# Optimization experiments

Hardware: AMD Instinct MI355X
Metric: run time of the kernel (lower is better)

Reference implementation:

```python
import jax, jax.numpy as jnp
import numpy as np
import math

HIDDEN_DIM = 1024
N_HEAD = 16
HEAD_DIM = HIDDEN_DIM // N_HEAD
BS, SEQ = 2, 4096


def setup_inputs() -> dict:
    key = jax.random.key(0)
    ks = jax.random.split(key, 6)
    s = 1.0 / math.sqrt(HIDDEN_DIM)
    return {
        "x": jax.random.normal(ks[0], (BS, SEQ, HIDDEN_DIM), dtype=jnp.float32),
        "attention_mask": jnp.zeros((1, 1, SEQ, SEQ), dtype=jnp.float32),
        "wq_w": jax.random.normal(ks[1], (HIDDEN_DIM, HIDDEN_DIM), dtype=jnp.float32) * s,
        "wq_b": jnp.zeros((HIDDEN_DIM,), dtype=jnp.float32),
        "wk_w": jax.random.normal(ks[2], (HIDDEN_DIM, HIDDEN_DIM), dtype=jnp.float32) * s,
        "wk_b": jnp.zeros((HIDDEN_DIM,), dtype=jnp.float32),
        "wv_w": jax.random.normal(ks[3], (HIDDEN_DIM, HIDDEN_DIM), dtype=jnp.float32) * s,
        "wv_b": jnp.zeros((HIDDEN_DIM,), dtype=jnp.float32),
        "wo_w": jax.random.normal(ks[4], (HIDDEN_DIM, HIDDEN_DIM), dtype=jnp.float32) * s,
        "wo_b": jnp.zeros((HIDDEN_DIM,), dtype=jnp.float32),
    }


def reference(x, attention_mask, wq_w, wq_b, wk_w, wk_b, wv_w, wv_b, wo_w, wo_b):
    bs, seq_len, _ = x.shape
    # nn.Linear: y = x @ W.T + b
    Q = x @ wq_w.T + wq_b
    K = x @ wk_w.T + wk_b
    V = x @ wv_w.T + wv_b
    # [bs, n_head, seq, head_dim]
    Q = Q.reshape(bs, seq_len, N_HEAD, HEAD_DIM).transpose(0, 2, 1, 3)
    K = K.reshape(bs, seq_len, N_HEAD, HEAD_DIM).transpose(0, 2, 1, 3)
    V = V.reshape(bs, seq_len, N_HEAD, HEAD_DIM).transpose(0, 2, 1, 3)
    scale = 1.0 / math.sqrt(HEAD_DIM)
    att = jnp.einsum('bhqd,bhkd->bhqk', Q, K) * scale
    att = att + attention_mask
    att = jax.nn.softmax(att, axis=-1)
    # dropout is identity in eval mode (p=0.1 during training)
    out = jnp.einsum('bhqk,bhkd->bhqd', att, V)
    out = out.transpose(0, 2, 1, 3).reshape(bs, seq_len, HIDDEN_DIM)
    return out @ wo_w.T + wo_b
```

## Files before the change

kernel.cpp:

```cpp
#include <hip/hip_runtime.h>

typedef unsigned short u16;
typedef __bf16 bf16x4 __attribute__((ext_vector_type(4)));
typedef __bf16 bf16x8 __attribute__((ext_vector_type(8)));
typedef float f32x4 __attribute__((ext_vector_type(4)));

#define SEQ_LEN 4096
#define HID 1024
#define NHEAD 16
#define HDIM 64
#define MROWS 8192
#define LOG2E 1.44269504088896f

__device__ __forceinline__ u16 f2bf(float f) {
  union { float f; unsigned u; } v; v.f = f;
  unsigned r = v.u + 0x7fffu + ((v.u >> 16) & 1u);
  return (u16)(r >> 16);
}

__device__ __forceinline__ float fexp2(float x) {
  float r;
  asm("v_exp_f32 %0, %1" : "=v"(r) : "v"(x));
  return r;
}

__device__ __forceinline__ void gload16(const void* g, void* lds) {
  __builtin_amdgcn_global_load_lds((const __attribute__((address_space(1))) void*)g,
                                   (__attribute__((address_space(3))) void*)lds, 16, 0, 0);
}


__global__ void cvt_x_kernel(const float* __restrict__ src, u16* __restrict__ dst, int n4) {
  int stride = gridDim.x * blockDim.x;
  for (int i = blockIdx.x * blockDim.x + threadIdx.x; i < n4; i += stride) {
    float4 v = ((const float4*)src)[i];
    ((ushort4*)dst)[i] = make_ushort4(f2bf(v.x), f2bf(v.y), f2bf(v.z), f2bf(v.w));
  }
}

__global__ void cvt_w_kernel(const float* __restrict__ w0, const float* __restrict__ w1,
                             const float* __restrict__ w2, const float* __restrict__ w3,
                             u16* __restrict__ dst) {
  const float* src = (blockIdx.y == 0) ? w0 : (blockIdx.y == 1) ? w1 : (blockIdx.y == 2) ? w2 : w3;
  u16* d = dst + (size_t)blockIdx.y * (HID * HID);
  int i = blockIdx.x * blockDim.x + threadIdx.x;
  float4 v = ((const float4*)src)[i];
  ((ushort4*)d)[i] = make_ushort4(f2bf(v.x), f2bf(v.y), f2bf(v.z), f2bf(v.w));
}

__global__ void maskchk_kernel(const float* __restrict__ mask, int n4, int* flag) {
  int stride = gridDim.x * blockDim.x;
  bool nz = false;
  for (int i = blockIdx.x * blockDim.x + threadIdx.x; i < n4; i += stride) {
    float4 v = ((const float4*)mask)[i];
    nz |= (v.x != 0.f) | (v.y != 0.f) | (v.z != 0.f) | (v.w != 0.f);
  }
  if (__any(nz) && (threadIdx.x & 63) == 0) atomicOr(flag, 1);
}


__device__ __forceinline__ void gemm_core(const u16* __restrict__ A, const u16* __restrict__ W,
                                          int m0, int n0, char* As, char* Bs, f32x4 acc[4][4]) {
  const int t = threadIdx.x, w = t >> 6, l = t & 63;
  const int lr = l & 15, lg = l >> 4;
  const int wr = (w >> 1) * 64, wc = (w & 1) * 64;
#pragma unroll
  for (int i = 0; i < 4; i++)
#pragma unroll
    for (int j = 0; j < 4; j++) acc[i][j] = (f32x4){0.f, 0.f, 0.f, 0.f};

  for (int k0 = 0; k0 < HID; k0 += 64) {
    __syncthreads();
#pragma unroll
    for (int j = 0; j < 4; j++) {
      int o = w * 4096 + j * 1024 + l * 16;
      int row = o >> 7, kb = (o >> 4) & 7, skb = kb ^ (row & 7);
      gload16(A + (size_t)(m0 + row) * HID + k0 + skb * 8, As + (w * 4096 + j * 1024));
      gload16(W + (size_t)(n0 + row) * HID + k0 + skb * 8, Bs + (w * 4096 + j * 1024));
    }
    __syncthreads();
#pragma unroll
    for (int ks = 0; ks < 2; ks++) {
      bf16x8 af[4], bf[4];
      int kb = ks * 4 + lg;
#pragma unroll
      for (int mt = 0; mt < 4; mt++) {
        int row = wr + mt * 16 + lr;
        af[mt] = *(const bf16x8*)(As + row * 128 + ((kb ^ (row & 7)) << 4));
      }
#pragma unroll
      for (int nt = 0; nt < 4; nt++) {
        int row = wc + nt * 16 + lr;
        bf[nt] = *(const bf16x8*)(Bs + row * 128 + ((kb ^ (row & 7)) << 4));
      }
#pragma unroll
      for (int mt = 0; mt < 4; mt++)
#pragma unroll
        for (int nt = 0; nt < 4; nt++)
          acc[mt][nt] = __builtin_amdgcn_mfma_f32_16x16x32_bf16(af[mt], bf[nt], acc[mt][nt], 0, 0, 0);
    }
  }
}

__global__ __launch_bounds__(256) void gemm_qkv_kernel(
    const u16* __restrict__ xb, const u16* __restrict__ wqb, const u16* __restrict__ wkb,
    const u16* __restrict__ wvb, const float* __restrict__ bq, const float* __restrict__ bk,
    const float* __restrict__ bv, u16* __restrict__ Qb, u16* __restrict__ Kb, u16* __restrict__ VT) {
  __shared__ __align__(128) char lds[32768];
  int m0 = blockIdx.x * 128;
  int ng = blockIdx.y * 128;
  int mat = ng >> 10, n0 = ng & 1023;
  const u16* W = (mat == 0) ? wqb : (mat == 1) ? wkb : wvb;
  const float* bias = (mat == 0) ? bq : (mat == 1) ? bk : bv;
  f32x4 acc[4][4];
  gemm_core(xb, W, m0, n0, lds, lds + 16384, acc);

  const int t = threadIdx.x, w = t >> 6, l = t & 63;
  const int lr = l & 15, lg = l >> 4;
  if (mat < 2) {
    u16* dst = (mat == 0) ? Qb : Kb;
    float scale = (mat == 0) ? 0.125f * LOG2E : 1.0f;
#pragma unroll
    for (int mt = 0; mt < 4; mt++)
#pragma unroll
      for (int nt = 0; nt < 4; nt++) {
        int n = n0 + (w & 1) * 64 + nt * 16 + lr;
        float bn = bias[n];
#pragma unroll
        for (int i = 0; i < 4; i++) {
          int m = m0 + (w >> 1) * 64 + mt * 16 + lg * 4 + i;
          dst[(size_t)m * HID + n] = f2bf((acc[mt][nt][i] + bn) * scale);
        }
      }
  } else {
#pragma unroll
    for (int mt = 0; mt < 4; mt++)
#pragma unroll
      for (int nt = 0; nt < 4; nt++) {
        int m = m0 + (w >> 1) * 64 + mt * 16 + lg * 4;
        int n = n0 + (w & 1) * 64 + nt * 16 + lr;
        int b = m >> 12, s = m & 4095;
        int h = n >> 6, d = n & 63;
        int t4 = (s >> 2) & 15;
        int t4p = ((t4 & 8)) | ((t4 & 3) << 1) | ((t4 >> 2) & 1);
        int sp = (s & ~63) | (t4p << 2);
        float bn = bias[n];
        ushort4 pk = make_ushort4(f2bf(acc[mt][nt][0] + bn), f2bf(acc[mt][nt][1] + bn),
                                  f2bf(acc[mt][nt][2] + bn), f2bf(acc[mt][nt][3] + bn));
        *(ushort4*)(VT + (((size_t)(b * NHEAD + h) * HDIM + d) * SEQ_LEN + sp)) = pk;
      }
  }
}

__global__ __launch_bounds__(256) void gemm_out_kernel(
    const u16* __restrict__ Ob, const u16* __restrict__ wob, const float* __restrict__ bo,
    float* __restrict__ out) {
  __shared__ __align__(128) char lds[32768];
  int m0 = blockIdx.x * 128, n0 = blockIdx.y * 128;
  f32x4 acc[4][4];
  gemm_core(Ob, wob, m0, n0, lds, lds + 16384, acc);
  const int t = threadIdx.x, w = t >> 6, l = t & 63;
  const int lr = l & 15, lg = l >> 4;
#pragma unroll
  for (int mt = 0; mt < 4; mt++)
#pragma unroll
    for (int nt = 0; nt < 4; nt++) {
      int n = n0 + (w & 1) * 64 + nt * 16 + lr;
      float bn = bo[n];
#pragma unroll
      for (int i = 0; i < 4; i++) {
        int m = m0 + (w >> 1) * 64 + mt * 16 + lg * 4 + i;
        out[(size_t)m * HID + n] = acc[mt][nt][i] + bn;
      }
    }
}

__global__ __launch_bounds__(512, 2) void attn_kernel(
    const u16* __restrict__ Qb, const u16* __restrict__ Kb, const u16* __restrict__ VT,
    const float* __restrict__ mask, const int* __restrict__ flag, u16* __restrict__ Ob) {
  __shared__ __align__(128) char lds[32768];
  const int flat = blockIdx.x;
  const int xcd = flat & 7;
  const int slot = flat >> 3;
  const int bh = xcd * 4 + (slot >> 5);
  const int bx = slot & 31;
  const int q0 = bx * 128;
  const int b = bh >> 4, h = bh & 15;
  const int t = threadIdx.x, w = t >> 6, l = t & 63;
  const int lr = l & 15, lg = l >> 4;
  const bool useMask = (flag[0] != 0);
  const int qrow = q0 + w * 16 + lr;

  const u16* qp = Qb + (size_t)(b * SEQ_LEN + qrow) * HID + h * HDIM;
  bf16x8 qf[2];
#pragma unroll
  for (int ks = 0; ks < 2; ks++) qf[ks] = *(const bf16x8*)(qp + (ks * 4 + lg) * 8);

  bf16x8 ones;
#pragma unroll
  for (int j = 0; j < 8; j++) ones[j] = (__bf16)1.0f;

  f32x4 oacc[4];
#pragma unroll
  for (int dt = 0; dt < 4; dt++) oacc[dt] = (f32x4){0.f, 0.f, 0.f, 0.f};
  f32x4 lacc = (f32x4){0.f, 0.f, 0.f, 0.f};
  float m_r = -1e30f;

  int off[2][4];
#pragma unroll
  for (int ks = 0; ks < 2; ks++) {
    int kb = ks * 4 + lg;
#pragma unroll
    for (int kt = 0; kt < 4; kt++) {
      int row = kt * 16 + lr;
      off[ks][kt] = row * 128 + ((kb ^ (row & 7)) << 4);
    }
  }

  const int o0 = t * 16;
  const int r0 = t >> 3;
  const int sk0 = (t & 7) ^ (r0 & 7);
  const u16* kg0 = Kb + (size_t)(b * SEQ_LEN) * HID + h * HDIM + (size_t)r0 * HID + sk0 * 8;
  const u16* vg0 = VT + ((size_t)(b * NHEAD + h) * HDIM + r0) * SEQ_LEN + sk0 * 8;

#define STAGE(BI)                                   \
  do {                                              \
    gload16(kg0, lds + (BI) * 8192 + o0);           \
    gload16(vg0, lds + 16384 + (BI) * 8192 + o0);   \
    kg0 += 64 * HID; vg0 += 64;                     \
  } while (0)

#define COMPUTE(BI, KV0)                                                                   \
  do {                                                                                     \
    const char* Ks = lds + (BI) * 8192;                                                    \
    const char* Vs = lds + 16384 + (BI) * 8192;                                            \
    f32x4 sf[4];                                                                           \
    _Pragma("unroll") for (int kt = 0; kt < 4; kt++) sf[kt] = (f32x4){0.f, 0.f, 0.f, 0.f}; \
    __builtin_amdgcn_s_setprio(1);                                                         \
    _Pragma("unroll") for (int ks = 0; ks < 2; ks++) {                                     \
      _Pragma("unroll") for (int kt = 0; kt < 4; kt++) {                                   \
        bf16x8 kf = *(const bf16x8*)(Ks + off[ks][kt]);                                    \
        sf[kt] = __builtin_amdgcn_mfma_f32_16x16x32_bf16(kf, qf[ks], sf[kt], 0, 0, 0);     \
      }                                                                                    \
    }                                                                                      \
    __builtin_amdgcn_s_setprio(0);                                                         \
    if (useMask) {                                                                         \
      _Pragma("unroll") for (int kt = 0; kt < 4; kt++)                                     \
      _Pragma("unroll") for (int i = 0; i < 4; i++)                                        \
          sf[kt][i] += mask[(size_t)qrow * SEQ_LEN + (KV0) + kt * 16 + lg * 4 + i] * LOG2E;\
    }                                                                                      \
    float mx = fmaxf(fmaxf(sf[0][0], sf[0][1]), sf[0][2]);                                 \
    mx = fmaxf(fmaxf(mx, sf[0][3]), sf[1][0]);                                             \
    mx = fmaxf(fmaxf(mx, sf[1][1]), sf[1][2]);                                             \
    mx = fmaxf(fmaxf(mx, sf[1][3]), sf[2][0]);                                             \
    mx = fmaxf(fmaxf(mx, sf[2][1]), sf[2][2]);                                             \
    mx = fmaxf(fmaxf(mx, sf[2][3]), sf[3][0]);                                             \
    mx = fmaxf(fmaxf(mx, sf[3][1]), sf[3][2]);                                             \
    mx = fmaxf(mx, sf[3][3]);                                                              \
    mx = fmaxf(mx, __shfl_xor(mx, 16));                                                    \
    mx = fmaxf(mx, __shfl_xor(mx, 32));                                                    \
    if (__any(mx > m_r + 8.0f)) {                                                          \
      float nm = fmaxf(m_r, mx);                                                           \
      float scf = fexp2(m_r - nm);                                                         \
      m_r = nm;                                                                            \
      _Pragma("unroll") for (int dt = 0; dt < 4; dt++)                                     \
      _Pragma("unroll") for (int i = 0; i < 4; i++) oacc[dt][i] *= scf;                    \
      lacc *= scf;                                                                         \
    }                                                                                      \
    _Pragma("unroll") for (int kt = 0; kt < 4; kt++)                                       \
    _Pragma("unroll") for (int i = 0; i < 4; i++) sf[kt][i] = fexp2(sf[kt][i] - m_r);      \
    _Pragma("unroll") for (int ks = 0; ks < 2; ks++) {                                     \
      bf16x8 pb;                                                                           \
      _Pragma("unroll") for (int j = 0; j < 4; j++) pb[j] = (__bf16)sf[2 * ks][j];         \
      _Pragma("unroll") for (int j = 0; j < 4; j++) pb[4 + j] = (__bf16)sf[2 * ks + 1][j]; \
      __builtin_amdgcn_s_setprio(1);                                                       \
      _Pragma("unroll") for (int dt = 0; dt < 4; dt++) {                                   \
        bf16x8 vf = *(const bf16x8*)(Vs + off[ks][dt]);                                    \
        oacc[dt] = __builtin_amdgcn_mfma_f32_16x16x32_bf16(vf, pb, oacc[dt], 0, 0, 0);     \
      }                                                                                    \
      lacc = __builtin_amdgcn_mfma_f32_16x16x32_bf16(ones, pb, lacc, 0, 0, 0);             \
      __builtin_amdgcn_s_setprio(0);                                                       \
    }                                                                                      \
  } while (0)

  STAGE(0);
  __syncthreads();

  const int NT = SEQ_LEN / 64;
  for (int t2 = 0; t2 < NT / 2; ++t2) {
    STAGE(1);
    COMPUTE(0, t2 * 128);
    __syncthreads();
    if (t2 != NT / 2 - 1) STAGE(0);
    COMPUTE(1, t2 * 128 + 64);
    __syncthreads();
  }
#undef STAGE
#undef COMPUTE

  float inv = 1.0f / lacc[0];
  u16* orow = Ob + (size_t)(b * SEQ_LEN + qrow) * HID + h * HDIM;
#pragma unroll
  for (int dt = 0; dt < 4; dt++) {
    ushort4 pk = make_ushort4(f2bf(oacc[dt][0] * inv), f2bf(oacc[dt][1] * inv),
                              f2bf(oacc[dt][2] * inv), f2bf(oacc[dt][3] * inv));
    *(ushort4*)(orow + dt * 16 + lg * 4) = pk;
  }
}


extern "C" void kernel_launch(void* const* d_in, const int* in_sizes, int n_in,
                              void* d_out, int out_size, void* d_ws, size_t ws_size,
                              hipStream_t stream) {
  const float* x    = (const float*)d_in[0];
  const float* mask = (const float*)d_in[1];
  const float* wq   = (const float*)d_in[2];
  const float* bq   = (const float*)d_in[3];
  const float* wk   = (const float*)d_in[4];
  const float* bk   = (const float*)d_in[5];
  const float* wv   = (const float*)d_in[6];
  const float* bv   = (const float*)d_in[7];
  const float* wo   = (const float*)d_in[8];
  const float* bo   = (const float*)d_in[9];

  char* ws = (char*)d_ws;
  u16* xb  = (u16*)(ws + 0);
  u16* wqb = (u16*)(ws + 16777216);
  u16* wkb = (u16*)(ws + 18874368);
  u16* wvb = (u16*)(ws + 20971520);
  u16* wob = (u16*)(ws + 23068672);
  u16* Qb  = (u16*)(ws + 25165824);
  u16* Kb  = (u16*)(ws + 41943040);
  u16* VT  = (u16*)(ws + 58720256);
  int* flag = (int*)(ws + 75497472);
  u16* Ob = xb;

  (void)hipMemsetAsync(flag, 0, 4, stream);
  cvt_x_kernel<<<2048, 256, 0, stream>>>(x, xb, MROWS * HID / 4);
  cvt_w_kernel<<<dim3(1024, 4), 256, 0, stream>>>(wq, wk, wv, wo, wqb);
  maskchk_kernel<<<2048, 256, 0, stream>>>(mask, SEQ_LEN * SEQ_LEN / 4, flag);
  gemm_qkv_kernel<<<dim3(64, 24), 256, 0, stream>>>(xb, wqb, wkb, wvb, bq, bk, bv, Qb, Kb, VT);
  attn_kernel<<<1024, 512, 0, stream>>>(Qb, Kb, VT, mask, flag, Ob);
  gemm_out_kernel<<<dim3(64, 8), 256, 0, stream>>>(Ob, wob, bo, (float*)d_out);
}
```

Baseline: 282.2 us.

## Process two query sub-tiles per wave in attention to reuse K/V LDS fragments

```diff
diff --git a/kernel.cpp b/kernel.cpp
--- a/kernel.cpp
+++ b/kernel.cpp
@@ -175,7 +175,7 @@
     }
 }
 
-__global__ __launch_bounds__(512, 2) void attn_kernel(
+__global__ __launch_bounds__(256, 2) void attn_kernel(
     const u16* __restrict__ Qb, const u16* __restrict__ Kb, const u16* __restrict__ VT,
     const float* __restrict__ mask, const int* __restrict__ flag, u16* __restrict__ Ob) {
   __shared__ __align__(128) char lds[32768];
@@ -189,22 +189,29 @@
   const int t = threadIdx.x, w = t >> 6, l = t & 63;
   const int lr = l & 15, lg = l >> 4;
   const bool useMask = (flag[0] != 0);
-  const int qrow = q0 + w * 16 + lr;
-
-  const u16* qp = Qb + (size_t)(b * SEQ_LEN + qrow) * HID + h * HDIM;
-  bf16x8 qf[2];
-#pragma unroll
-  for (int ks = 0; ks < 2; ks++) qf[ks] = *(const bf16x8*)(qp + (ks * 4 + lg) * 8);
+  int qrow[2];
+#pragma unroll
+  for (int s = 0; s < 2; s++) qrow[s] = q0 + (w * 2 + s) * 16 + lr;
+
+  bf16x8 qf[2][2];
+#pragma unroll
+  for (int s = 0; s < 2; s++) {
+    const u16* qp = Qb + (size_t)(b * SEQ_LEN + qrow[s]) * HID + h * HDIM;
+#pragma unroll
+    for (int ks = 0; ks < 2; ks++) qf[s][ks] = *(const bf16x8*)(qp + (ks * 4 + lg) * 8);
+  }
 
   bf16x8 ones;
 #pragma unroll
   for (int j = 0; j < 8; j++) ones[j] = (__bf16)1.0f;
 
-  f32x4 oacc[4];
-#pragma unroll
-  for (int dt = 0; dt < 4; dt++) oacc[dt] = (f32x4){0.f, 0.f, 0.f, 0.f};
-  f32x4 lacc = (f32x4){0.f, 0.f, 0.f, 0.f};
-  float m_r = -1e30f;
+  f32x4 oacc[2][4];
+#pragma unroll
+  for (int s = 0; s < 2; s++)
+#pragma unroll
+    for (int dt = 0; dt < 4; dt++) oacc[s][dt] = (f32x4){0.f, 0.f, 0.f, 0.f};
+  f32x4 lacc[2] = {(f32x4){0.f, 0.f, 0.f, 0.f}, (f32x4){0.f, 0.f, 0.f, 0.f}};
+  float m_r[2] = {-1e30f, -1e30f};
 
   int off[2][4];
 #pragma unroll
@@ -218,69 +225,94 @@
   }
 
   const int o0 = t * 16;
+  const int o1 = o0 + 4096;
   const int r0 = t >> 3;
+  const int r1 = r0 + 32;
   const int sk0 = (t & 7) ^ (r0 & 7);
+  const int sk1 = (t & 7) ^ (r1 & 7);
   const u16* kg0 = Kb + (size_t)(b * SEQ_LEN) * HID + h * HDIM + (size_t)r0 * HID + sk0 * 8;
+  const u16* kg1 = Kb + (size_t)(b * SEQ_LEN) * HID + h * HDIM + (size_t)r1 * HID + sk1 * 8;
   const u16* vg0 = VT + ((size_t)(b * NHEAD + h) * HDIM + r0) * SEQ_LEN + sk0 * 8;
-
-#define STAGE(BI)                                   \
-  do {                                              \
-    gload16(kg0, lds + (BI) * 8192 + o0);           \
-    gload16(vg0, lds + 16384 + (BI) * 8192 + o0);   \
-    kg0 += 64 * HID; vg0 += 64;                     \
+  const u16* vg1 = VT + ((size_t)(b * NHEAD + h) * HDIM + r1) * SEQ_LEN + sk1 * 8;
+
+#define STAGE(BI)                                            \
+  do {                                                       \
+    gload16(kg0, lds + (BI) * 8192 + o0);                    \
+    gload16(kg1, lds + (BI) * 8192 + o1);                    \
+    gload16(vg0, lds + 16384 + (BI) * 8192 + o0);            \
+    gload16(vg1, lds + 16384 + (BI) * 8192 + o1);            \
+    kg0 += 64 * HID; kg1 += 64 * HID; vg0 += 64; vg1 += 64;  \
   } while (0)
 
 #define COMPUTE(BI, KV0)                                                                   \
   do {                                                                                     \
     const char* Ks = lds + (BI) * 8192;                                                    \
     const char* Vs = lds + 16384 + (BI) * 8192;                                            \
-    f32x4 sf[4];                                                                           \
-    _Pragma("unroll") for (int kt = 0; kt < 4; kt++) sf[kt] = (f32x4){0.f, 0.f, 0.f, 0.f}; \
+    bf16x8 kf[2][4];                                                                       \
+    _Pragma("unroll") for (int ks = 0; ks < 2; ks++)                                       \
+    _Pragma("unroll") for (int kt = 0; kt < 4; kt++)                                       \
+        kf[ks][kt] = *(const bf16x8*)(Ks + off[ks][kt]);                                   \
+    f32x4 sf[2][4];                                                                        \
+    _Pragma("unroll") for (int s = 0; s < 2; s++)                                          \
+    _Pragma("unroll") for (int kt = 0; kt < 4; kt++) sf[s][kt] = (f32x4){0.f,0.f,0.f,0.f}; \
     __builtin_amdgcn_s_setprio(1);                                                         \
-    _Pragma("unroll") for (int ks = 0; ks < 2; ks++) {                                     \
-      _Pragma("unroll") for (int kt = 0; kt < 4; kt++) {                                   \
-        bf16x8 kf = *(const bf16x8*)(Ks + off[ks][kt]);                                    \
-        sf[kt] = __builtin_amdgcn_mfma_f32_16x16x32_bf16(kf, qf[ks], sf[kt], 0, 0, 0);     \
+    _Pragma("unroll") for (int ks = 0; ks < 2; ks++)                                       \
+    _Pragma("unroll") for (int s = 0; s < 2; s++)                                          \
+    _Pragma("unroll") for (int kt = 0; kt < 4; kt++)                                       \
+        sf[s][kt] = __builtin_amdgcn_mfma_f32_16x16x32_bf16(kf[ks][kt], qf[s][ks],         \
+                                                            sf[s][kt], 0, 0, 0);          \
+    __builtin_amdgcn_s_setprio(0);                                                         \
+    if (useMask) {                                                                         \
+      _Pragma("unroll") for (int s = 0; s < 2; s++)                                        \
+      _Pragma("unroll") for (int kt = 0; kt < 4; kt++)                                     \
+      _Pragma("unroll") for (int i = 0; i < 4; i++)                                        \
+          sf[s][kt][i] +=                                                                  \
+              mask[(size_t)qrow[s] * SEQ_LEN + (KV0) + kt * 16 + lg * 4 + i] * LOG2E;      \
+    }                                                                                      \
+    float mx[2];                                                                           \
+    _Pragma("unroll") for (int s = 0; s < 2; s++) {                                        \
+      float m1 = fmaxf(fmaxf(sf[s][0][0], sf[s][0][1]), sf[s][0][2]);                      \
+      m1 = fmaxf(fmaxf(m1, sf[s][0][3]), sf[s][1][0]);                                     \
+      m1 = fmaxf(fmaxf(m1, sf[s][1][1]), sf[s][1][2]);                                     \
+      m1 = fmaxf(fmaxf(m1, sf[s][1][3]), sf[s][2][0]);                                     \
+      m1 = fmaxf(fmaxf(m1, sf[s][2][1]), sf[s][2][2]);                                     \
+      m1 = fmaxf(fmaxf(m1, sf[s][2][3]), sf[s][3][0]);                                     \
+      m1 = fmaxf(fmaxf(m1, sf[s][3][1]), sf[s][3][2]);                                     \
+      m1 = fmaxf(m1, sf[s][3][3]);                                                         \
+      m1 = fmaxf(m1, __shfl_xor(m1, 16));                                                  \
+      mx[s] = fmaxf(m1, __shfl_xor(m1, 32));                                               \
+    }                                                                                      \
+    if (__any(fmaxf(mx[0] - m_r[0], mx[1] - m_r[1]) > 8.0f)) {                             \
+      _Pragma("unroll") for (int s = 0; s < 2; s++) {                                      \
+        float nm = fmaxf(m_r[s], mx[s]);                                                   \
+        float scf = fexp2(m_r[s] - nm);                                                    \
+        m_r[s] = nm;                                                                       \
+        _Pragma("unroll") for (int dt = 0; dt < 4; dt++)                                   \
+        _Pragma("unroll") for (int i = 0; i < 4; i++) oacc[s][dt][i] *= scf;               \
+        lacc[s] *= scf;                                                                    \
+      }                                                                                    \
+    }                                                                                      \
+    _Pragma("unroll") for (int s = 0; s < 2; s++)                                          \
+    _Pragma("unroll") for (int kt = 0; kt < 4; kt++)                                       \
+    _Pragma("unroll") for (int i = 0; i < 4; i++)                                          \
+        sf[s][kt][i] = fexp2(sf[s][kt][i] - m_r[s]);                                       \
+    bf16x8 vf[2][4];                                                                       \
+    _Pragma("unroll") for (int ks = 0; ks < 2; ks++)                                       \
+    _Pragma("unroll") for (int dt = 0; dt < 4; dt++)                                       \
+        vf[ks][dt] = *(const bf16x8*)(Vs + off[ks][dt]);                                   \
+    __builtin_amdgcn_s_setprio(1);                                                         \
+    _Pragma("unroll") for (int s = 0; s < 2; s++) {                                        \
+      _Pragma("unroll") for (int ks = 0; ks < 2; ks++) {                                   \
+        bf16x8 pb;                                                                         \
+        _Pragma("unroll") for (int j = 0; j < 4; j++) pb[j] = (__bf16)sf[s][2 * ks][j];    \
+        _Pragma("unroll") for (int j = 0; j < 4; j++) pb[4 + j] = (__bf16)sf[s][2*ks+1][j];\
+        _Pragma("unroll") for (int dt = 0; dt < 4; dt++)                                   \
+            oacc[s][dt] =                                                                  \
+                __builtin_amdgcn_mfma_f32_16x16x32_bf16(vf[ks][dt], pb, oacc[s][dt],0,0,0);\
+        lacc[s] = __builtin_amdgcn_mfma_f32_16x16x32_bf16(ones, pb, lacc[s], 0, 0, 0);     \
       }                                                                                    \
     }                                                                                      \
     __builtin_amdgcn_s_setprio(0);                                                         \
-    if (useMask) {                                                                         \
-      _Pragma("unroll") for (int kt = 0; kt < 4; kt++)                                     \
-      _Pragma("unroll") for (int i = 0; i < 4; i++)                                        \
-          sf[kt][i] += mask[(size_t)qrow * SEQ_LEN + (KV0) + kt * 16 + lg * 4 + i] * LOG2E;\
-    }                                                                                      \
-    float mx = fmaxf(fmaxf(sf[0][0], sf[0][1]), sf[0][2]);                                 \
-    mx = fmaxf(fmaxf(mx, sf[0][3]), sf[1][0]);                                             \
-    mx = fmaxf(fmaxf(mx, sf[1][1]), sf[1][2]);                                             \
-    mx = fmaxf(fmaxf(mx, sf[1][3]), sf[2][0]);                                             \
-    mx = fmaxf(fmaxf(mx, sf[2][1]), sf[2][2]);                                             \
-    mx = fmaxf(fmaxf(mx, sf[2][3]), sf[3][0]);                                             \
-    mx = fmaxf(fmaxf(mx, sf[3][1]), sf[3][2]);                                             \
-    mx = fmaxf(mx, sf[3][3]);                                                              \
-    mx = fmaxf(mx, __shfl_xor(mx, 16));                                                    \
-    mx = fmaxf(mx, __shfl_xor(mx, 32));                                                    \
-    if (__any(mx > m_r + 8.0f)) {                                                          \
-      float nm = fmaxf(m_r, mx);                                                           \
-      float scf = fexp2(m_r - nm);                                                         \
-      m_r = nm;                                                                            \
-      _Pragma("unroll") for (int dt = 0; dt < 4; dt++)                                     \
-      _Pragma("unroll") for (int i = 0; i < 4; i++) oacc[dt][i] *= scf;                    \
-      lacc *= scf;                                                                         \
-    }                                                                                      \
-    _Pragma("unroll") for (int kt = 0; kt < 4; kt++)                                       \
-    _Pragma("unroll") for (int i = 0; i < 4; i++) sf[kt][i] = fexp2(sf[kt][i] - m_r);      \
-    _Pragma("unroll") for (int ks = 0; ks < 2; ks++) {                                     \
-      bf16x8 pb;                                                                           \
-      _Pragma("unroll") for (int j = 0; j < 4; j++) pb[j] = (__bf16)sf[2 * ks][j];         \
-      _Pragma("unroll") for (int j = 0; j < 4; j++) pb[4 + j] = (__bf16)sf[2 * ks + 1][j]; \
-      __builtin_amdgcn_s_setprio(1);                                                       \
-      _Pragma("unroll") for (int dt = 0; dt < 4; dt++) {                                   \
-        bf16x8 vf = *(const bf16x8*)(Vs + off[ks][dt]);                                    \
-        oacc[dt] = __builtin_amdgcn_mfma_f32_16x16x32_bf16(vf, pb, oacc[dt], 0, 0, 0);     \
-      }                                                                                    \
-      lacc = __builtin_amdgcn_mfma_f32_16x16x32_bf16(ones, pb, lacc, 0, 0, 0);             \
-      __builtin_amdgcn_s_setprio(0);                                                       \
-    }                                                                                      \
   } while (0)
 
   STAGE(0);
@@ -298,13 +330,16 @@
 #undef STAGE
 #undef COMPUTE
 
-  float inv = 1.0f / lacc[0];
-  u16* orow = Ob + (size_t)(b * SEQ_LEN + qrow) * HID + h * HDIM;
-#pragma unroll
-  for (int dt = 0; dt < 4; dt++) {
-    ushort4 pk = make_ushort4(f2bf(oacc[dt][0] * inv), f2bf(oacc[dt][1] * inv),
-                              f2bf(oacc[dt][2] * inv), f2bf(oacc[dt][3] * inv));
-    *(ushort4*)(orow + dt * 16 + lg * 4) = pk;
+#pragma unroll
+  for (int s = 0; s < 2; s++) {
+    float inv = 1.0f / lacc[s][0];
+    u16* orow = Ob + (size_t)(b * SEQ_LEN + qrow[s]) * HID + h * HDIM;
+#pragma unroll
+    for (int dt = 0; dt < 4; dt++) {
+      ushort4 pk = make_ushort4(f2bf(oacc[s][dt][0] * inv), f2bf(oacc[s][dt][1] * inv),
+                                f2bf(oacc[s][dt][2] * inv), f2bf(oacc[s][dt][3] * inv));
+      *(ushort4*)(orow + dt * 16 + lg * 4) = pk;
+    }
   }
 }
 
@@ -340,6 +375,6 @@
   cvt_w_kernel<<<dim3(1024, 4), 256, 0, stream>>>(wq, wk, wv, wo, wqb);
   maskchk_kernel<<<2048, 256, 0, stream>>>(mask, SEQ_LEN * SEQ_LEN / 4, flag);
   gemm_qkv_kernel<<<dim3(64, 24), 256, 0, stream>>>(xb, wqb, wkb, wvb, bq, bk, bv, Qb, Kb, VT);
-  attn_kernel<<<1024, 512, 0, stream>>>(Qb, Kb, VT, mask, flag, Ob);
+  attn_kernel<<<1024, 256, 0, stream>>>(Qb, Kb, VT, mask, flag, Ob);
   gemm_out_kernel<<<dim3(64, 8), 256, 0, stream>>>(Ob, wob, bo, (float*)d_out);
 }
```

New measurement: 276.0 us. -2.2%, faster.
